# Performance work log

Hardware: AMD Instinct MI355X
Metric: run time of the kernel (lower is better)

Reference implementation:

```python
import jax, jax.numpy as jnp
import numpy as np

B, SEQ, VOCAB = 128, 200, 1400
D = 256          # input_size == hidden_size
H = 256
NCLS = 128


def _p(key, shape, scale=0.05):
    return jax.random.normal(key, shape, dtype=jnp.float32) * scale


def setup_inputs() -> dict:
    key = jax.random.key(0)
    ks = jax.random.split(key, 24)
    inp = {
        "inputs": jax.random.uniform(ks[0], (B, SEQ, VOCAB), dtype=jnp.float32),
        "timestamps": jax.random.uniform(ks[1], (B, SEQ), dtype=jnp.float32),
        "emb": _p(ks[2], (VOCAB, D)),
        # TimeLSTM 1
        "Wall1_w": _p(ks[3], (4 * H, D)), "Wall1_b": _p(ks[4], (4 * H,)),
        "Uall1_w": _p(ks[5], (4 * H, H)), "Uall1_b": _p(ks[6], (4 * H,)),
        "Wd1_w": _p(ks[7], (H, H)), "Wd1_b": _p(ks[8], (H,)),
        # TimeLSTM 2
        "Wall2_w": _p(ks[9], (4 * H, D)), "Wall2_b": _p(ks[10], (4 * H,)),
        "Uall2_w": _p(ks[11], (4 * H, H)), "Uall2_b": _p(ks[12], (4 * H,)),
        "Wd2_w": _p(ks[13], (H, H)), "Wd2_b": _p(ks[14], (H,)),
        # attention / output heads
        "wa_w": _p(ks[15], (1, H)),
        "Wb_w": _p(ks[16], (H, H)),
        "Wout_w": _p(ks[17], (NCLS, H)),
        # initial states (torch.randn in original forward)
        "h01": jax.random.normal(ks[18], (B, H), dtype=jnp.float32),
        "c01": jax.random.normal(ks[19], (B, H), dtype=jnp.float32),
        "h02": jax.random.normal(ks[20], (B, H), dtype=jnp.float32),
        "c02": jax.random.normal(ks[21], (B, H), dtype=jnp.float32),
    }
    return inp


def _time_lstm(embedded, timestamps, h0, c0, Wall_w, Wall_b, Uall_w, Uall_b, Wd_w, Wd_b):
    # Precompute the input projection for all steps (one big GEMM).
    # NOTE: original code applies W_all to h and U_all to x.
    ux = jnp.einsum('bsd,ed->sbe', embedded, Uall_w) + Uall_b  # [seq, b, 4h]
    ts = jnp.swapaxes(timestamps, 0, 1)[:, :, None]            # [seq, b, 1]

    def step(carry, xs):
        h, c = carry
        ux_s, t_s = xs
        c_s1 = jnp.tanh(c @ Wd_w.T + Wd_b)
        c_adj = c - c_s1 + c_s1 * t_s
        gates = jax.nn.sigmoid(h @ Wall_w.T + Wall_b + ux_s)   # all 4 gates sigmoid (incl. c_tmp)
        f, i, o, c_tmp = jnp.split(gates, 4, axis=1)
        c_new = f * c_adj + i * c_tmp
        h_new = o * jnp.tanh(c_new)
        return (h_new, c_new), h_new

    _, hs = jax.lax.scan(step, (h0, c0), (ux, ts))
    return jnp.swapaxes(hs, 0, 1)  # [b, seq, h]


def reference(inputs, timestamps, emb,
              Wall1_w, Wall1_b, Uall1_w, Uall1_b, Wd1_w, Wd1_b,
              Wall2_w, Wall2_b, Uall2_w, Uall2_b, Wd2_w, Wd2_b,
              wa_w, Wb_w, Wout_w, h01, c01, h02, c02):
    embedded = jnp.einsum('bsv,vd->bsd', inputs, emb)  # [b, seq, d]
    out1 = _time_lstm(embedded, timestamps, h01, c01,
                      Wall1_w, Wall1_b, Uall1_w, Uall1_b, Wd1_w, Wd1_b)
    E = jnp.einsum('bsh,h->bs', out1, wa_w[0])
    alpha = jax.nn.softmax(E, axis=1)                  # [b, seq]
    out2 = _time_lstm(embedded, timestamps, h02, c02,
                      Wall2_w, Wall2_b, Uall2_w, Uall2_b, Wd2_w, Wd2_b)
    Beta = jnp.tanh(jnp.einsum('bsh,kh->bsk', out2, Wb_w))  # [b, seq, h]
    ctx = jnp.sum(embedded * Beta * alpha[:, :, None], axis=1)  # [b, h]
    return ctx @ Wout_w.T  # [b, num_classes]
```

## Files before the change

kernel.cpp:

```cpp
#include <hip/hip_runtime.h>

typedef unsigned short u16;
typedef unsigned long long u64;
typedef __attribute__((ext_vector_type(8))) short bf16x8;
typedef __attribute__((ext_vector_type(4))) float f32x4;
typedef __attribute__((ext_vector_type(4))) unsigned short us4;

#define MFMA(a,b,c) __builtin_amdgcn_mfma_f32_16x16x32_bf16((a),(b),(c),0,0,0)
#define KEEP(x) asm volatile("" : "+v"(x))


static __device__ __forceinline__ u16 f2b(float f){
  unsigned u = __float_as_uint(f);
  u += 0x7fffu + ((u >> 16) & 1u);
  return (u16)(u >> 16);
}
static __device__ __forceinline__ float sigm(float x){ return 1.0f/(1.0f+__expf(-x)); }
static __device__ __forceinline__ float tanhx(float x){
  x = fminf(fmaxf(x, -15.f), 15.f);
  float e = __expf(-2.f*x);
  return (1.f - e)/(1.f + e);
}
static __device__ __forceinline__ void gl16(const void* g, void* l){
  __builtin_amdgcn_global_load_lds((const __attribute__((address_space(1))) void*)g,
                                   (__attribute__((address_space(3))) void*)l, 16, 0, 0);
}

__global__ __launch_bounds__(256) void k_prep(
  const float* __restrict__ in0, u16* __restrict__ A0,
  const float* __restrict__ emb, u16* __restrict__ embT,
  const float* __restrict__ s0, const float* __restrict__ s1, const float* __restrict__ s2,
  const float* __restrict__ s3, const float* __restrict__ s4, const float* __restrict__ s5,
  const float* __restrict__ s6,
  u16* __restrict__ d0, u16* __restrict__ d1, u16* __restrict__ d2, u16* __restrict__ d3,
  u16* __restrict__ d4, u16* __restrict__ d5, u16* __restrict__ d6)
{
  int bx = blockIdx.x, tid = threadIdx.x;
  if (bx < 35200){
    long long i4 = (long long)bx*256 + tid;
    long long o = i4*4;
    int r = (int)(o / 1408);
    int c = (int)(o % 1408);
    us4 d;
    if (c + 4 <= 1400){
      f32x4 v = *(const f32x4*)&in0[(long long)r*1400 + c];
      d[0]=f2b(v[0]); d[1]=f2b(v[1]); d[2]=f2b(v[2]); d[3]=f2b(v[3]);
    } else {
      for (int k=0;k<4;k++){ int cc=c+k; d[k] = (cc<1400)? f2b(in0[(long long)r*1400+cc]) : (u16)0; }
    }
    *(us4*)&A0[(long long)r*1408 + c] = d;
  } else if (bx < 36608){
    int idx = (bx-35200)*256 + tid;
    int n = idx / 1408, k = idx % 1408;
    embT[idx] = (k < 1400) ? f2b(emb[(long long)k*256 + n]) : (u16)0;
  } else {
    long long q = (long long)(bx-36608)*256 + tid;
    const float* src; u16* dst; long long rel;
    if      (q < 65536)  { src=s0; dst=d0; rel=q; }
    else if (q < 131072) { src=s1; dst=d1; rel=q-65536; }
    else if (q < 196608) { src=s2; dst=d2; rel=q-131072; }
    else if (q < 262144) { src=s3; dst=d3; rel=q-196608; }
    else if (q < 278528) { src=s4; dst=d4; rel=q-262144; }
    else if (q < 294912) { src=s5; dst=d5; rel=q-278528; }
    else                 { src=s6; dst=d6; rel=q-294912; }
    long long o = rel*4;
    f32x4 v = *(const f32x4*)&src[o];
    us4 d; d[0]=f2b(v[0]); d[1]=f2b(v[1]); d[2]=f2b(v[2]); d[3]=f2b(v[3]);
    *(us4*)&dst[o] = d;
  }
}

__global__ __launch_bounds__(256) void k_init(float* __restrict__ E, float* __restrict__ ctx){
  int i = blockIdx.x*256 + threadIdx.x;
  if (i < 25600) E[i] = 0.f;
  else ctx[i-25600] = 0.f;
}

template<int EPI>
__global__ __launch_bounds__(256) void k_gemm(const u16* __restrict__ A, const u16* __restrict__ Bt,
    int N, int K,
    float* __restrict__ Cf, u16* __restrict__ Cb,
    const float* __restrict__ bias1, const float* __restrict__ bias2,
    const u16* __restrict__ Bt2, float* __restrict__ Cf2,
    const float* __restrict__ bias3, const float* __restrict__ bias4,
    const float* __restrict__ emb, const float* __restrict__ alpha)
{
  __shared__ __align__(16) u16 As[128*64];
  __shared__ __align__(16) u16 Bs[128*64];
  __shared__ float red[2][128];
  const int tid = threadIdx.x;
  const int l = tid & 63, w = tid >> 6;
  const int quad = l >> 4, lb = l & 15;
  const int wr = w >> 1, wc = w & 1;
  const long long m0 = (long long)blockIdx.x * 128;
  int n0 = blockIdx.y * 128;
  if (EPI==4 && blockIdx.y >= 8){
    Bt = Bt2; Cf = Cf2; bias1 = bias3; bias2 = bias4; n0 = (blockIdx.y-8)*128;
  }

  f32x4 acc[4][4];
  #pragma unroll
  for (int i=0;i<4;i++)
    #pragma unroll
    for (int j=0;j<4;j++) acc[i][j] = (f32x4){0.f,0.f,0.f,0.f};

  for (int kk = 0; kk < K; kk += 64){
    #pragma unroll
    for (int it=0; it<4; ++it){
      int slot = it*256 + tid;
      int m = slot >> 3;
      int q = (slot & 7) ^ (m & 7);
      gl16(A + (m0+m)*K + kk + q*8, &As[slot*8]);
    }
    #pragma unroll
    for (int it=0; it<4; ++it){
      int slot = it*256 + tid;
      int m = slot >> 3;
      int q = (slot & 7) ^ (m & 7);
      gl16(Bt + (long long)(n0+m)*K + kk + q*8, &Bs[slot*8]);
    }
    __syncthreads();
    #pragma unroll
    for (int ks=0; ks<2; ++ks){
      int kq = quad + ks*4;
      bf16x8 af[4], bfr[4];
      #pragma unroll
      for (int i=0;i<4;i++){ int m = wr*64 + i*16 + lb; af[i]  = *(const bf16x8*)&As[m*64 + ((kq ^ (m&7))*8)]; }
      #pragma unroll
      for (int j=0;j<4;j++){ int n = wc*64 + j*16 + lb; bfr[j] = *(const bf16x8*)&Bs[n*64 + ((kq ^ (n&7))*8)]; }
      #pragma unroll
      for (int i=0;i<4;i++)
        #pragma unroll
        for (int j=0;j<4;j++)
          acc[i][j] = MFMA(af[i], bfr[j], acc[i][j]);
    }
    __syncthreads();
  }

  if (EPI==5){
    const int b0 = (int)(m0 / 200);
    red[tid>>7][tid&127] = 0.f;
    __syncthreads();
    #pragma unroll
    for (int i=0;i<4;i++){
      #pragma unroll
      for (int j=0;j<4;j++){
        int col = wc*64 + j*16 + lb;
        #pragma unroll
        for (int r=0;r<4;r++){
          long long row = m0 + wr*64 + i*16 + quad*4 + r;
          long long o = row*N + n0 + col;
          float v = emb[o] * tanhx(acc[i][j][r]) * alpha[row];
          atomicAdd(&red[(int)(row/200) - b0][col], v);
        }
      }
    }
    __syncthreads();
    int bl = tid >> 7, col = tid & 127;
    int bb = b0 + bl;
    if (bb < 128) atomicAdd(&Cf[bb*256 + n0 + col], red[bl][col]);
    return;
  }

  #pragma unroll
  for (int i=0;i<4;i++){
    #pragma unroll
    for (int j=0;j<4;j++){
      int col = n0 + wc*64 + j*16 + lb;
      #pragma unroll
      for (int r=0;r<4;r++){
        long long row = m0 + wr*64 + i*16 + quad*4 + r;
        long long o = row*N + col;
        float v = acc[i][j][r];
        if (EPI==1){ Cf[o]=v; Cb[o]=f2b(v); }
        else { Cf[o] = v + bias1[col] + bias2[col]; }
      }
    }
  }
}

__global__ __launch_bounds__(256,1) void k_scan(
  const u16* __restrict__ Wall1, const u16* __restrict__ Wd1, const float* __restrict__ Wd1b,
  const float* __restrict__ ux1, const float* __restrict__ h01, const float* __restrict__ c01,
  const u16* __restrict__ Wall2, const u16* __restrict__ Wd2, const float* __restrict__ Wd2b,
  const float* __restrict__ ux2, const float* __restrict__ h02, const float* __restrict__ c02,
  const float* __restrict__ ts, const float* __restrict__ wa,
  float* __restrict__ E, u16* __restrict__ out2,
  u16* __restrict__ hx, u16* __restrict__ cx, int* __restrict__ seqw)
{
  __shared__ __align__(16) u16 hb[16][264];
  __shared__ __align__(16) u16 cb[16][264];
  const int bi = blockIdx.x;
  const int lstm = bi >> 5;
  const int bc   = (bi >> 2) & 7;
  const int jw   = bi & 3;
  const int grp  = bi >> 2;
  const u16* Wall  = lstm ? Wall2 : Wall1;
  const u16* Wd    = lstm ? Wd2   : Wd1;
  const float* Wdb = lstm ? Wd2b  : Wd1b;
  const float* ux  = lstm ? ux2   : ux1;
  const float* h0  = lstm ? h02   : h01;
  const float* c0  = lstm ? c02   : c01;

  const int tid = threadIdx.x;
  const int l = tid & 63, w = tid >> 6;
  const int quad = l >> 4, lb = l & 15;
  const int bg = bc*16 + lb;
  const int jwave = jw*64 + w*16;
  const int jlane = jwave + quad*4;
  const int bb = tid >> 4, jj = tid & 15, j0 = jj*16;
  const int wjw = jj >> 2;

  bf16x8 wfA[4][8], wdA[8];
  #pragma unroll
  for (int g=0; g<4; ++g)
    #pragma unroll
    for (int kk=0; kk<8; ++kk){
      wfA[g][kk] = *(const bf16x8*)&Wall[(long long)(g*256 + jwave + lb)*256 + kk*32 + quad*8];
      KEEP(wfA[g][kk]);
    }
  #pragma unroll
  for (int kk=0; kk<8; ++kk){
    wdA[kk] = *(const bf16x8*)&Wd[(long long)(jwave + lb)*256 + kk*32 + quad*8];
    KEEP(wdA[kk]);
  }

  f32x4 bcs  = *(const f32x4*)&Wdb[jlane];
  f32x4 wav  = *(const f32x4*)&wa[jlane];
  f32x4 creg = *(const f32x4*)&c0[(long long)bg*256 + jlane];

  {
    #pragma unroll
    for (int kq=0; kq<4; ++kq){
      f32x4 hv = *(const f32x4*)&h0[(long long)(bc*16+bb)*256 + j0 + kq*4];
      f32x4 cv = *(const f32x4*)&c0[(long long)(bc*16+bb)*256 + j0 + kq*4];
      us4 hp, cp;
      #pragma unroll
      for (int r=0;r<4;++r){ hp[r]=f2b(hv[r]); cp[r]=f2b(cv[r]); }
      *(us4*)&hb[bb][j0+kq*4] = hp;
      *(us4*)&cb[bb][j0+kq*4] = cp;
    }
  }
  __syncthreads();

  f32x4 uxr[4];
  #pragma unroll
  for (int g=0; g<4; ++g)
    uxr[g] = *(const f32x4*)&ux[(long long)bg*200*1024 + g*256 + jlane];
  float tcur = ts[(long long)bg*200];

  for (int s=0; s<200; ++s){
    f32x4 ad = bcs;
    #pragma unroll
    for (int kk=0;kk<8;++kk){
      bf16x8 cf = *(const bf16x8*)&cb[lb][kk*32 + quad*8];
      ad = MFMA(wdA[kk], cf, ad);
    }
    f32x4 ag[4];
    #pragma unroll
    for (int g=0; g<4; ++g) ag[g] = uxr[g];
    #pragma unroll
    for (int kk=0;kk<8;++kk){
      bf16x8 hf = *(const bf16x8*)&hb[lb][kk*32 + quad*8];
      #pragma unroll
      for (int g=0; g<4; ++g) ag[g] = MFMA(wfA[g][kk], hf, ag[g]);
    }
    f32x4 hn; us4 hp, cp;
    #pragma unroll
    for (int r=0;r<4;++r){
      float cs1 = tanhx(ad[r]);
      float cadj = creg[r] + cs1*(tcur - 1.0f);
      float fg = sigm(ag[0][r]);
      float ig = sigm(ag[1][r]);
      float og = sigm(ag[2][r]);
      float cg = sigm(ag[3][r]);
      float cn = fg*cadj + ig*cg;
      float hv = og*tanhx(cn);
      creg[r]=cn; hn[r]=hv;
      hp[r]=f2b(hv); cp[r]=f2b(cn);
    }
    if (lstm==0){
      float e = hn[0]*wav[0] + hn[1]*wav[1] + hn[2]*wav[2] + hn[3]*wav[3];
      e += __shfl_xor(e, 16, 64);
      e += __shfl_xor(e, 32, 64);
      if (l < 16) atomicAdd(&E[(long long)bg*200 + s], e);
    } else {
      *(us4*)&out2[((long long)bg*200 + s)*256 + jlane] = hp;
    }
    if (s < 199){
      const int slot = (s+1)&1;
      u64 hv64, cv64;
      __builtin_memcpy(&hv64,&hp,8); __builtin_memcpy(&cv64,&cp,8);
      long long xbase = ((long long)(slot*16 + grp)*16 + lb)*256 + jlane;
      __hip_atomic_store((u64*)&hx[xbase], hv64, __ATOMIC_RELAXED, __HIP_MEMORY_SCOPE_AGENT);
      __hip_atomic_store((u64*)&cx[xbase], cv64, __ATOMIC_RELAXED, __HIP_MEMORY_SCOPE_AGENT);
      __syncthreads();
      if (tid == 0)
        __hip_atomic_store(&seqw[(slot*16+grp)*4 + jw], s+1, __ATOMIC_RELAXED, __HIP_MEMORY_SCOPE_AGENT);
      #pragma unroll
      for (int g=0; g<4; ++g)
        uxr[g] = *(const f32x4*)&ux[((long long)bg*200 + s+1)*1024 + g*256 + jlane];
      float tnext = ts[(long long)bg*200 + s+1];
      *(us4*)&hb[lb][jlane] = hp;
      *(us4*)&cb[lb][jlane] = cp;
      if (wjw != jw){
        const int* sp = &seqw[(slot*16+grp)*4 + wjw];
        while (__hip_atomic_load(sp, __ATOMIC_RELAXED, __HIP_MEMORY_SCOPE_AGENT) != s+1)
          __builtin_amdgcn_s_sleep(1);
        long long rbase = ((long long)(slot*16 + grp)*16 + bb)*256 + j0;
        u64 hvv[4], cvv[4];
        #pragma unroll
        for (int kq=0;kq<4;++kq){
          hvv[kq] = __hip_atomic_load((const u64*)&hx[rbase + kq*4], __ATOMIC_RELAXED, __HIP_MEMORY_SCOPE_AGENT);
          cvv[kq] = __hip_atomic_load((const u64*)&cx[rbase + kq*4], __ATOMIC_RELAXED, __HIP_MEMORY_SCOPE_AGENT);
        }
        #pragma unroll
        for (int kq=0;kq<4;++kq){
          *(u64*)&hb[bb][j0+kq*4] = hvv[kq];
          *(u64*)&cb[bb][j0+kq*4] = cvv[kq];
        }
      }
      tcur = tnext;
      __syncthreads();
    }
  }
}

__global__ __launch_bounds__(256) void k_attn(const float* __restrict__ E, float* __restrict__ alpha){
  __shared__ float buf[256];
  int b = blockIdx.x, tid = threadIdx.x;
  float Ev = (tid < 200) ? E[(long long)b*200 + tid] : -1e30f;
  buf[tid]=Ev; __syncthreads();
  for (int st=128; st>0; st>>=1){ if (tid<st) buf[tid]=fmaxf(buf[tid],buf[tid+st]); __syncthreads(); }
  float mx = buf[0]; __syncthreads();
  float e = (tid<200)? __expf(Ev-mx) : 0.f;
  buf[tid]=e; __syncthreads();
  for (int st=128; st>0; st>>=1){ if (tid<st) buf[tid]+=buf[tid+st]; __syncthreads(); }
  float sm = buf[0];
  if (tid<200) alpha[(long long)b*200+tid] = e/sm;
}

__global__ __launch_bounds__(128) void k_out(const float* __restrict__ ctx, const float* __restrict__ Wout,
                                             float* __restrict__ out){
  __shared__ float cs[256];
  int b = blockIdx.x, t = threadIdx.x;
  cs[t] = ctx[b*256+t]; cs[t+128] = ctx[b*256+t+128];
  __syncthreads();
  const float* wr = Wout + (long long)t*256;
  float a0=0,a1=0,a2=0,a3=0;
  for (int j=0;j<256;j+=4){
    f32x4 v = *(const f32x4*)&wr[j];
    a0+=v[0]*cs[j]; a1+=v[1]*cs[j+1]; a2+=v[2]*cs[j+2]; a3+=v[3]*cs[j+3];
  }
  out[(long long)b*128 + t] = (a0+a1)+(a2+a3);
}

extern "C" void kernel_launch(void* const* d_in, const int* in_sizes, int n_in,
                              void* d_out, int out_size, void* d_ws, size_t ws_size,
                              hipStream_t stream)
{
  (void)in_sizes; (void)n_in; (void)out_size; (void)ws_size;
  const float* inputs = (const float*)d_in[0];
  const float* tstamp = (const float*)d_in[1];
  const float* emb    = (const float*)d_in[2];
  const float* Wall1w = (const float*)d_in[3];
  const float* Wall1b = (const float*)d_in[4];
  const float* Uall1w = (const float*)d_in[5];
  const float* Uall1b = (const float*)d_in[6];
  const float* Wd1w   = (const float*)d_in[7];
  const float* Wd1b   = (const float*)d_in[8];
  const float* Wall2w = (const float*)d_in[9];
  const float* Wall2b = (const float*)d_in[10];
  const float* Uall2w = (const float*)d_in[11];
  const float* Uall2b = (const float*)d_in[12];
  const float* Wd2w   = (const float*)d_in[13];
  const float* Wd2b   = (const float*)d_in[14];
  const float* wa     = (const float*)d_in[15];
  const float* Wbw    = (const float*)d_in[16];
  const float* Woutw  = (const float*)d_in[17];
  const float* h01    = (const float*)d_in[18];
  const float* c01    = (const float*)d_in[19];
  const float* h02    = (const float*)d_in[20];
  const float* c02    = (const float*)d_in[21];

  char* ws = (char*)d_ws;
  float* ux1   = (float*)(ws + 0);
  float* ux2   = (float*)(ws + 104857600LL);
  float* embF  = (float*)(ws + 209715200LL);
  u16*   embB  = (u16*)  (ws + 235929600LL);
  char*  scr   =          ws + 249036800LL;
  u16*   A0    = (u16*)scr;
  u16*   out2  = (u16*)  (scr + 0);
  float* alpha = (float*)(scr + 39321600LL);
  float* ctx   = (float*)(scr + 39424000LL);
  float* E     = (float*)(scr + 39555072LL);
  u16*   hx    = (u16*)  (scr + 39657472LL);
  u16*   cx    = (u16*)  (scr + 39919616LL);
  int*   seqw  = (int*)  (scr + 40181760LL);
  u16* embT    = (u16*)(ws + 321126400LL);
  u16* Wall1B  = (u16*)(ws + 321847296LL);
  u16* Wall2B  = (u16*)(ws + 322371584LL);
  u16* Uall1B  = (u16*)(ws + 322895872LL);
  u16* Uall2B  = (u16*)(ws + 323420160LL);
  u16* Wd1B    = (u16*)(ws + 323944448LL);
  u16* Wd2B    = (u16*)(ws + 324075520LL);
  u16* WbB     = (u16*)(ws + 324206592LL);

  k_prep<<<37824, 256, 0, stream>>>(inputs, A0, emb, embT,
                                    Wall1w, Wall2w, Uall1w, Uall2w, Wd1w, Wd2w, Wbw,
                                    Wall1B, Wall2B, Uall1B, Uall2B, Wd1B, Wd2B, WbB);
  k_gemm<1><<<dim3(200,2), 256, 0, stream>>>(A0, embT, 256, 1408, embF, embB,
                                             nullptr, nullptr, nullptr, nullptr,
                                             nullptr, nullptr, nullptr, nullptr);
  k_gemm<4><<<dim3(200,16), 256, 0, stream>>>(embB, Uall1B, 1024, 256, ux1, nullptr,
                                              Uall1b, Wall1b,
                                              Uall2B, ux2, Uall2b, Wall2b,
                                              nullptr, nullptr);
  k_init<<<228, 256, 0, stream>>>(E, ctx);
  k_scan<<<64, 256, 0, stream>>>(Wall1B, Wd1B, Wd1b, ux1, h01, c01,
                                 Wall2B, Wd2B, Wd2b, ux2, h02, c02,
                                 tstamp, wa, E, out2, hx, cx, seqw);
  k_attn<<<128, 256, 0, stream>>>(E, alpha);
  k_gemm<5><<<dim3(200,2), 256, 0, stream>>>(out2, WbB, 256, 256, ctx, nullptr,
                                             nullptr, nullptr, nullptr, nullptr,
                                             nullptr, nullptr, embF, alpha);
  k_out<<<128, 128, 0, stream>>>(ctx, Woutw, (float*)d_out);
}
```

Before: 1.138 ms.

## Replace flag-based cross-block handoff with tagged data words in scan

```diff
diff --git a/kernel.cpp b/kernel.cpp
--- a/kernel.cpp
+++ b/kernel.cpp
@@ -1,6 +1,7 @@
 #include <hip/hip_runtime.h>
 
 typedef unsigned short u16;
+typedef unsigned int u32;
 typedef unsigned long long u64;
 typedef __attribute__((ext_vector_type(8))) short bf16x8;
 typedef __attribute__((ext_vector_type(4))) float f32x4;
@@ -186,15 +187,15 @@
   const float* __restrict__ ux2, const float* __restrict__ h02, const float* __restrict__ c02,
   const float* __restrict__ ts, const float* __restrict__ wa,
   float* __restrict__ E, u16* __restrict__ out2,
-  u16* __restrict__ hx, u16* __restrict__ cx, int* __restrict__ seqw)
+  u64* __restrict__ hx, u64* __restrict__ cx)
 {
   __shared__ __align__(16) u16 hb[16][264];
   __shared__ __align__(16) u16 cb[16][264];
   const int bi = blockIdx.x;
-  const int lstm = bi >> 5;
-  const int bc   = (bi >> 2) & 7;
-  const int jw   = bi & 3;
-  const int grp  = bi >> 2;
+  const int jw   = bi >> 4;
+  const int grp  = bi & 15;
+  const int lstm = (bi >> 3) & 1;
+  const int bc   = bi & 7;
   const u16* Wall  = lstm ? Wall2 : Wall1;
   const u16* Wd    = lstm ? Wd2   : Wd1;
   const float* Wdb = lstm ? Wd2b  : Wd1b;
@@ -250,15 +251,22 @@
   float tcur = ts[(long long)bg*200];
 
   for (int s=0; s<200; ++s){
+    const float tnow = tcur;
     f32x4 ad = bcs;
+    f32x4 ag[4];
+    #pragma unroll
+    for (int g=0; g<4; ++g) ag[g] = uxr[g];
+    if (s < 199){
+      #pragma unroll
+      for (int g=0; g<4; ++g)
+        uxr[g] = *(const f32x4*)&ux[((long long)bg*200 + s+1)*1024 + g*256 + jlane];
+      tcur = ts[(long long)bg*200 + s+1];
+    }
     #pragma unroll
     for (int kk=0;kk<8;++kk){
       bf16x8 cf = *(const bf16x8*)&cb[lb][kk*32 + quad*8];
       ad = MFMA(wdA[kk], cf, ad);
     }
-    f32x4 ag[4];
-    #pragma unroll
-    for (int g=0; g<4; ++g) ag[g] = uxr[g];
     #pragma unroll
     for (int kk=0;kk<8;++kk){
       bf16x8 hf = *(const bf16x8*)&hb[lb][kk*32 + quad*8];
@@ -269,7 +277,7 @@
     #pragma unroll
     for (int r=0;r<4;++r){
       float cs1 = tanhx(ad[r]);
-      float cadj = creg[r] + cs1*(tcur - 1.0f);
+      float cadj = creg[r] + cs1*(tnow - 1.0f);
       float fg = sigm(ag[0][r]);
       float ig = sigm(ag[1][r]);
       float og = sigm(ag[2][r]);
@@ -289,39 +297,50 @@
     }
     if (s < 199){
       const int slot = (s+1)&1;
-      u64 hv64, cv64;
-      __builtin_memcpy(&hv64,&hp,8); __builtin_memcpy(&cv64,&cp,8);
-      long long xbase = ((long long)(slot*16 + grp)*16 + lb)*256 + jlane;
-      __hip_atomic_store((u64*)&hx[xbase], hv64, __ATOMIC_RELAXED, __HIP_MEMORY_SCOPE_AGENT);
-      __hip_atomic_store((u64*)&cx[xbase], cv64, __ATOMIC_RELAXED, __HIP_MEMORY_SCOPE_AGENT);
-      __syncthreads();
-      if (tid == 0)
-        __hip_atomic_store(&seqw[(slot*16+grp)*4 + jw], s+1, __ATOMIC_RELAXED, __HIP_MEMORY_SCOPE_AGENT);
-      #pragma unroll
-      for (int g=0; g<4; ++g)
-        uxr[g] = *(const f32x4*)&ux[((long long)bg*200 + s+1)*1024 + g*256 + jlane];
-      float tnext = ts[(long long)bg*200 + s+1];
+      const u32 tag = 0x6B390000u + (u32)(s+1);
+      {
+        u64 th0 = ((u64)tag<<32) | (u32)((u32)hp[0] | ((u32)hp[1]<<16));
+        u64 th1 = ((u64)tag<<32) | (u32)((u32)hp[2] | ((u32)hp[3]<<16));
+        u64 tc0 = ((u64)tag<<32) | (u32)((u32)cp[0] | ((u32)cp[1]<<16));
+        u64 tc1 = ((u64)tag<<32) | (u32)((u32)cp[2] | ((u32)cp[3]<<16));
+        long long xb = ((long long)(slot*16 + grp)*16 + lb)*128 + (jlane>>1);
+        __hip_atomic_store(&hx[xb],   th0, __ATOMIC_RELAXED, __HIP_MEMORY_SCOPE_AGENT);
+        __hip_atomic_store(&hx[xb+1], th1, __ATOMIC_RELAXED, __HIP_MEMORY_SCOPE_AGENT);
+        __hip_atomic_store(&cx[xb],   tc0, __ATOMIC_RELAXED, __HIP_MEMORY_SCOPE_AGENT);
+        __hip_atomic_store(&cx[xb+1], tc1, __ATOMIC_RELAXED, __HIP_MEMORY_SCOPE_AGENT);
+      }
+      asm volatile("" ::: "memory");
+      __builtin_amdgcn_s_barrier();
+      asm volatile("" ::: "memory");
       *(us4*)&hb[lb][jlane] = hp;
       *(us4*)&cb[lb][jlane] = cp;
       if (wjw != jw){
-        const int* sp = &seqw[(slot*16+grp)*4 + wjw];
-        while (__hip_atomic_load(sp, __ATOMIC_RELAXED, __HIP_MEMORY_SCOPE_AGENT) != s+1)
+        long long rb = ((long long)(slot*16 + grp)*16 + bb)*128 + (j0>>1);
+        u64 hv[8], cv[8];
+        for (;;){
+          #pragma unroll
+          for (int k=0;k<8;++k)
+            hv[k] = __hip_atomic_load(&hx[rb+k], __ATOMIC_RELAXED, __HIP_MEMORY_SCOPE_AGENT);
+          #pragma unroll
+          for (int k=0;k<8;++k)
+            cv[k] = __hip_atomic_load(&cx[rb+k], __ATOMIC_RELAXED, __HIP_MEMORY_SCOPE_AGENT);
+          bool ok = true;
+          #pragma unroll
+          for (int k=0;k<8;++k)
+            ok = ok && ((u32)(hv[k]>>32) == tag) && ((u32)(cv[k]>>32) == tag);
+          if (ok) break;
           __builtin_amdgcn_s_sleep(1);
-        long long rbase = ((long long)(slot*16 + grp)*16 + bb)*256 + j0;
-        u64 hvv[4], cvv[4];
-        #pragma unroll
-        for (int kq=0;kq<4;++kq){
-          hvv[kq] = __hip_atomic_load((const u64*)&hx[rbase + kq*4], __ATOMIC_RELAXED, __HIP_MEMORY_SCOPE_AGENT);
-          cvv[kq] = __hip_atomic_load((const u64*)&cx[rbase + kq*4], __ATOMIC_RELAXED, __HIP_MEMORY_SCOPE_AGENT);
         }
         #pragma unroll
-        for (int kq=0;kq<4;++kq){
-          *(u64*)&hb[bb][j0+kq*4] = hvv[kq];
-          *(u64*)&cb[bb][j0+kq*4] = cvv[kq];
+        for (int k=0;k<4;++k){
+          *(u64*)&hb[bb][j0 + 4*k] = (u64)(u32)hv[2*k] | ((u64)(u32)hv[2*k+1] << 32);
+          *(u64*)&cb[bb][j0 + 4*k] = (u64)(u32)cv[2*k] | ((u64)(u32)cv[2*k+1] << 32);
         }
       }
-      tcur = tnext;
-      __syncthreads();
+      asm volatile("s_waitcnt lgkmcnt(0)" ::: "memory");
+      __builtin_amdgcn_sched_barrier(0);
+      __builtin_amdgcn_s_barrier();
+      asm volatile("" ::: "memory");
     }
   }
 }
@@ -394,9 +413,8 @@
   float* alpha = (float*)(scr + 39321600LL);
   float* ctx   = (float*)(scr + 39424000LL);
   float* E     = (float*)(scr + 39555072LL);
-  u16*   hx    = (u16*)  (scr + 39657472LL);
-  u16*   cx    = (u16*)  (scr + 39919616LL);
-  int*   seqw  = (int*)  (scr + 40181760LL);
+  u64*   hx    = (u64*)  (scr + 39657472LL);
+  u64*   cx    = (u64*)  (scr + 40181760LL);
   u16* embT    = (u16*)(ws + 321126400LL);
   u16* Wall1B  = (u16*)(ws + 321847296LL);
   u16* Wall2B  = (u16*)(ws + 322371584LL);
@@ -419,7 +437,7 @@
   k_init<<<228, 256, 0, stream>>>(E, ctx);
   k_scan<<<64, 256, 0, stream>>>(Wall1B, Wd1B, Wd1b, ux1, h01, c01,
                                  Wall2B, Wd2B, Wd2b, ux2, h02, c02,
-                                 tstamp, wa, E, out2, hx, cx, seqw);
+                                 tstamp, wa, E, out2, hx, cx);
   k_attn<<<128, 256, 0, stream>>>(E, alpha);
   k_gemm<5><<<dim3(200,2), 256, 0, stream>>>(out2, WbB, 256, 256, ctx, nullptr,
                                              nullptr, nullptr, nullptr, nullptr,
```

New measurement: 1.374 ms. 20.8% more time.
